# Performance work log

Measured on AMD Instinct MI355X. Metric: run time of the kernel, lower is better.

The kernel has to match this reference:

```python
import jax, jax.numpy as jnp
import numpy as np

D_MODEL = 2048
NUM_HEADS = 32
NUM_GROUPS = 8
D_K = D_MODEL // NUM_HEADS          # 64
HPG = NUM_HEADS // NUM_GROUPS       # heads per group = 4
B, S = 2, 2048


def setup_inputs() -> dict:
    key = jax.random.key(0)
    ks = jax.random.split(key, 9)
    w_scale = 0.02
    kv_dim = NUM_GROUPS * D_K
    return {
        "x":  jax.random.normal(ks[0], (B, S, D_MODEL), dtype=jnp.float32),
        "Wq": jax.random.normal(ks[1], (D_MODEL, D_MODEL), dtype=jnp.float32) * w_scale,
        "bq": jnp.zeros((D_MODEL,), dtype=jnp.float32),
        "Wk": jax.random.normal(ks[2], (D_MODEL, kv_dim), dtype=jnp.float32) * w_scale,
        "bk": jnp.zeros((kv_dim,), dtype=jnp.float32),
        "Wv": jax.random.normal(ks[3], (D_MODEL, kv_dim), dtype=jnp.float32) * w_scale,
        "bv": jnp.zeros((kv_dim,), dtype=jnp.float32),
        "Wo": jax.random.normal(ks[4], (D_MODEL, D_MODEL), dtype=jnp.float32) * w_scale,
        "bo": jnp.zeros((D_MODEL,), dtype=jnp.float32),
    }


def reference(x, Wq, bq, Wk, bk, Wv, bv, Wo, bo):
    b, s, _ = x.shape
    # projections (torch Linear math: x @ W^T + b, here weights stored as (in,out))
    Q = (x @ Wq + bq).reshape(b, s, NUM_HEADS, D_K).transpose(0, 2, 1, 3)   # [B,H,S,dk]
    Kg = (x @ Wk + bk).reshape(b, s, NUM_GROUPS, D_K).transpose(0, 2, 1, 3)  # [B,G,S,dk]
    Vg = (x @ Wv + bv).reshape(b, s, NUM_GROUPS, D_K).transpose(0, 2, 1, 3)
    # repeat_interleave K/V over head dim to full head count
    K = jnp.repeat(Kg, HPG, axis=1)  # [B,H,S,dk]
    V = jnp.repeat(Vg, HPG, axis=1)
    scores = jnp.einsum("bhqd,bhkd->bhqk", Q, K) / np.sqrt(D_K).astype(np.float32)
    attn = jax.nn.softmax(scores, axis=-1)
    out = jnp.einsum("bhqk,bhkd->bhqd", attn, V)               # [B,H,S,dk]
    out = out.transpose(0, 2, 1, 3).reshape(b, s, D_MODEL)
    out = out @ Wo + bo
    # module returns grouped K,V cache: K[:, ::HPG] == Kg
    return out, (Kg, Vg)
```

## Files before the change

### kernel.cpp

```cpp
#include <hip/hip_runtime.h>
#include <hip/hip_bf16.h>
#include <stdint.h>

#define S_LEN 2048
#define DM    2048
#define NH    32
#define NG    8
#define DK    64
#define BATCH 2
#define MROWS (BATCH*S_LEN)
#define NQKV  3072
#define SSCALE 0.18033688f

typedef __bf16 bf16x8 __attribute__((ext_vector_type(8)));
typedef short  s16x8  __attribute__((ext_vector_type(8)));
typedef float  f32x4  __attribute__((ext_vector_type(4)));
typedef unsigned int u32x4 __attribute__((ext_vector_type(4)));

__device__ __forceinline__ unsigned short f2b(float f) {
    unsigned int x = __float_as_uint(f);
    unsigned int r = (x + 0x7fffu + ((x >> 16) & 1u)) >> 16;
    return (unsigned short)r;
}
__device__ __forceinline__ bf16x8 ld8(const unsigned short* p) {
    return *(const bf16x8*)p;
}
__device__ __forceinline__ s16x8 cvt8(const float* p) {
    f32x4 a = *(const f32x4*)p;
    f32x4 b = *(const f32x4*)(p + 4);
    s16x8 o;
#pragma unroll
    for (int j = 0; j < 4; j++) { o[j] = (short)f2b(a[j]); o[4 + j] = (short)f2b(b[j]); }
    return o;
}
__device__ __forceinline__ void gl_lds(const unsigned short* g, unsigned short* l) {
    __builtin_amdgcn_global_load_lds(
        (const __attribute__((address_space(1))) unsigned int*)g,
        (__attribute__((address_space(3))) unsigned int*)l, 16, 0, 0);
}
__device__ __forceinline__ void wait_dma() {
    asm volatile("s_waitcnt vmcnt(0)" ::: "memory");
}

__global__ __launch_bounds__(256) void cvt_x(const float* __restrict__ in,
                                             unsigned short* __restrict__ out) {
    size_t id = (size_t)blockIdx.x * 256 + threadIdx.x;
    *(s16x8*)&out[id * 8] = cvt8(in + id * 8);
}

__global__ void transpose_cvt(const float* __restrict__ in,
                              unsigned short* __restrict__ out, int R, int C) {
    __shared__ float t[32][33];
    int c0 = blockIdx.x * 32, r0 = blockIdx.y * 32;
    int tx = threadIdx.x, ty = threadIdx.y;
#pragma unroll
    for (int i = 0; i < 4; i++)
        t[ty + i * 8][tx] = in[(size_t)(r0 + ty + i * 8) * C + c0 + tx];
    __syncthreads();
#pragma unroll
    for (int i = 0; i < 4; i++)
        out[(size_t)(c0 + ty + i * 8) * R + r0 + tx] = f2b(t[tx][ty + i * 8]);
}

__global__ void bias_concat(const float* __restrict__ bq, const float* __restrict__ bk,
                            const float* __restrict__ bv, float* __restrict__ o) {
    int i = blockIdx.x * 256 + threadIdx.x;
    if (i < 2048) o[i] = bq[i];
    else if (i < 2560) o[i] = bk[i - 2048];
    else if (i < 3072) o[i] = bv[i - 2560];
}

__global__ __launch_bounds__(256, 4) void gemm_qkv(const unsigned short* __restrict__ A,
                                                const unsigned short* __restrict__ Bt,
                                                const float* __restrict__ bias,
                                                unsigned short* __restrict__ Qb,
                                                float* __restrict__ Kg, float* __restrict__ Vg,
                                                unsigned short* __restrict__ Kb,
                                                unsigned short* __restrict__ Vtb) {
    __shared__ alignas(16) unsigned short As[2][128 * 32];
    __shared__ alignas(16) unsigned short Bs[2][128 * 32];
    const int K = DM;
    const int tid = threadIdx.x;
    const int n0 = blockIdx.x * 128, m0 = blockIdx.y * 128;
    const int w = tid >> 6, lane = tid & 63;
    const int ln15 = lane & 15, quad = lane >> 4;
    const int wm = (w >> 1) * 64, wn = (w & 1) * 64;
    const int xq = (quad ^ ((ln15 >> 1) & 3)) * 8;
    f32x4 acc[4][4] = {};

#define GSTAGE(k0v, buf) do {                                                    \
    _Pragma("unroll")                                                            \
    for (int i = 0; i < 2; ++i) {                                                \
        int s = w * 128 + i * 64 + lane;             \
        int r = s >> 2, cb = (s & 3) ^ ((r >> 1) & 3);                           \
        gl_lds(&A[(size_t)(m0 + r) * K + (k0v) + cb * 8],                        \
               &As[buf][(w * 128 + i * 64) * 8]);                                \
        gl_lds(&Bt[(size_t)(n0 + r) * K + (k0v) + cb * 8],                       \
               &Bs[buf][(w * 128 + i * 64) * 8]);                                \
    } } while (0)

    GSTAGE(0, 0);
    wait_dma();
    __syncthreads();
    int cur = 0;
    for (int k0 = 0; k0 < K; k0 += 32) {
        if (k0 + 32 < K) GSTAGE(k0 + 32, cur ^ 1);
        bf16x8 af[4], bfr[4];
#pragma unroll
        for (int mt = 0; mt < 4; mt++)
            af[mt] = ld8(&As[cur][(wm + mt * 16 + ln15) * 32 + xq]);
#pragma unroll
        for (int nt = 0; nt < 4; nt++)
            bfr[nt] = ld8(&Bs[cur][(wn + nt * 16 + ln15) * 32 + xq]);
        __builtin_amdgcn_s_setprio(1);
#pragma unroll
        for (int mt = 0; mt < 4; mt++)
#pragma unroll
            for (int nt = 0; nt < 4; nt++)
                acc[mt][nt] = __builtin_amdgcn_mfma_f32_16x16x32_bf16(af[mt], bfr[nt], acc[mt][nt], 0, 0, 0);
        __builtin_amdgcn_s_setprio(0);
        wait_dma();
        __syncthreads();
        cur ^= 1;
    }
#undef GSTAGE
#pragma unroll
    for (int nt = 0; nt < 4; nt++) {
        int col = n0 + wn + nt * 16 + ln15;
        float bv = bias[col];
#pragma unroll
        for (int mt = 0; mt < 4; mt++) {
            int row0 = m0 + wm + mt * 16 + quad * 4;
#pragma unroll
            for (int r = 0; r < 4; r++) {
                float val = acc[mt][nt][r] + bv;
                int row = row0 + r;
                int b = row >> 11, s = row & 2047;
                if (col < 2048) {
                    Qb[(size_t)row * DM + col] = f2b(val * SSCALE);
                } else if (col < 2560) {
                    int gc = col - 2048, g = gc >> 6, d = gc & 63;
                    size_t idx = (((size_t)(b * NG + g) * S_LEN + s) << 6) + d;
                    Kg[idx] = val;
                    Kb[idx] = f2b(val);
                } else {
                    int gc = col - 2560, g = gc >> 6, d = gc & 63;
                    Vg[(((size_t)(b * NG + g) * S_LEN + s) << 6) + d] = val;
                    Vtb[((size_t)(b * NG + g) * DK + d) * S_LEN + s] = f2b(val);
                }
            }
        }
    }
}

__global__ __launch_bounds__(256, 4) void gemm_o(const unsigned short* __restrict__ A,
                                              const unsigned short* __restrict__ Bt,
                                              const float* __restrict__ bias,
                                              float* __restrict__ C) {
    __shared__ alignas(16) unsigned short As[2][128 * 32];
    __shared__ alignas(16) unsigned short Bs[2][128 * 32];
    const int K = DM, N = DM;
    const int tid = threadIdx.x;
    const int n0 = blockIdx.x * 128, m0 = blockIdx.y * 128;
    const int w = tid >> 6, lane = tid & 63;
    const int ln15 = lane & 15, quad = lane >> 4;
    const int wm = (w >> 1) * 64, wn = (w & 1) * 64;
    const int xq = (quad ^ ((ln15 >> 1) & 3)) * 8;
    f32x4 acc[4][4] = {};

#define GSTAGE(k0v, buf) do {                                                    \
    _Pragma("unroll")                                                            \
    for (int i = 0; i < 2; ++i) {                                                \
        int s = w * 128 + i * 64 + lane;                                         \
        int r = s >> 2, cb = (s & 3) ^ ((r >> 1) & 3);                           \
        gl_lds(&A[(size_t)(m0 + r) * K + (k0v) + cb * 8],                        \
               &As[buf][(w * 128 + i * 64) * 8]);                                \
        gl_lds(&Bt[(size_t)(n0 + r) * K + (k0v) + cb * 8],                       \
               &Bs[buf][(w * 128 + i * 64) * 8]);                                \
    } } while (0)

    GSTAGE(0, 0);
    wait_dma();
    __syncthreads();
    int cur = 0;
    for (int k0 = 0; k0 < K; k0 += 32) {
        if (k0 + 32 < K) GSTAGE(k0 + 32, cur ^ 1);
        bf16x8 af[4], bfr[4];
#pragma unroll
        for (int mt = 0; mt < 4; mt++)
            af[mt] = ld8(&As[cur][(wm + mt * 16 + ln15) * 32 + xq]);
#pragma unroll
        for (int nt = 0; nt < 4; nt++)
            bfr[nt] = ld8(&Bs[cur][(wn + nt * 16 + ln15) * 32 + xq]);
        __builtin_amdgcn_s_setprio(1);
#pragma unroll
        for (int mt = 0; mt < 4; mt++)
#pragma unroll
            for (int nt = 0; nt < 4; nt++)
                acc[mt][nt] = __builtin_amdgcn_mfma_f32_16x16x32_bf16(af[mt], bfr[nt], acc[mt][nt], 0, 0, 0);
        __builtin_amdgcn_s_setprio(0);
        wait_dma();
        __syncthreads();
        cur ^= 1;
    }
#undef GSTAGE
#pragma unroll
    for (int nt = 0; nt < 4; nt++) {
        int col = n0 + wn + nt * 16 + ln15;
        float bv = bias[col];
#pragma unroll
        for (int mt = 0; mt < 4; mt++) {
            int row0 = m0 + wm + mt * 16 + quad * 4;
#pragma unroll
            for (int r = 0; r < 4; r++)
                C[(size_t)(row0 + r) * N + col] = acc[mt][nt][r] + bv;
        }
    }
}

#define MT 2
__global__ __launch_bounds__(256, 4) void attn_fwd(const unsigned short* __restrict__ Qb,
                                                   const unsigned short* __restrict__ Kb,
                                                   const unsigned short* __restrict__ Vtb,
                                                   unsigned short* __restrict__ AO) {
    __shared__ alignas(16) unsigned short Ks[2][64 * 64];
    __shared__ alignas(16) unsigned short Vt[2][64 * 64];
    const int b = blockIdx.z, h = blockIdx.y, q0 = blockIdx.x * (MT * 64);
    const int g = h >> 2;
    const int tid = threadIdx.x;
    const int w = tid >> 6, lane = tid & 63;
    const int ln15 = lane & 15, quad = lane >> 4;
    const int x7a = (quad ^ (ln15 & 7)) * 8;
    const int x7b = x7a ^ 32;

    bf16x8 aq[MT][2];
#pragma unroll
    for (int mt = 0; mt < MT; mt++) {
        const size_t qrow =
            ((size_t)(b * S_LEN + q0 + w * (MT * 16) + mt * 16 + ln15)) * DM + h * DK;
        aq[mt][0] = ld8(&Qb[qrow + quad * 8]);
        aq[mt][1] = ld8(&Qb[qrow + 32 + quad * 8]);
    }

    bf16x8 ones;
#pragma unroll
    for (int j = 0; j < 8; j++) ones[j] = (__bf16)1.0f;

    f32x4 o[MT][4] = {};
    f32x4 l_acc[MT] = {};
    const size_t kvb = ((size_t)(b * NG + g)) * S_LEN * DK;

#define STAGE(k0v, buf) do {                                                     \
    _Pragma("unroll")                                                            \
    for (int i = 0; i < 2; i++) {                                                \
        int s = w * 128 + i * 64 + lane;                                         \
        int r = s >> 3, cb = (s & 7) ^ (r & 7);                                  \
        gl_lds(&Kb[kvb + (size_t)((k0v) + r) * DK + cb * 8],                     \
               &Ks[buf][(w * 128 + i * 64) * 8]);                                \
        gl_lds(&Vtb[kvb + (size_t)r * S_LEN + (k0v) + cb * 8],                   \
               &Vt[buf][(w * 128 + i * 64) * 8]);                                \
    } } while (0)

    STAGE(0, 0);
    wait_dma();
    __syncthreads();
    int cur = 0;

    for (int k0 = 0; k0 < S_LEN; k0 += 64) {
        if (k0 + 64 < S_LEN) STAGE(k0 + 64, cur ^ 1);

        f32x4 z[MT][4];
        __builtin_amdgcn_s_setprio(1);
#pragma unroll
        for (int nt = 0; nt < 4; nt++) {
            bf16x8 bk0 = ld8(&Ks[cur][(nt * 16 + ln15) * 64 + x7a]);
            bf16x8 bk1 = ld8(&Ks[cur][(nt * 16 + ln15) * 64 + x7b]);
#pragma unroll
            for (int mt = 0; mt < MT; mt++) {
                f32x4 t = {0.f, 0.f, 0.f, 0.f};
                t = __builtin_amdgcn_mfma_f32_16x16x32_bf16(bk0, aq[mt][0], t, 0, 0, 0);
                t = __builtin_amdgcn_mfma_f32_16x16x32_bf16(bk1, aq[mt][1], t, 0, 0, 0);
                z[mt][nt] = t;
            }
        }
        __builtin_amdgcn_s_setprio(0);

        bf16x8 pa[MT][2];
#pragma unroll
        for (int mt = 0; mt < MT; mt++) {
            unsigned int S[4][2];
#pragma unroll
            for (int nt = 0; nt < 4; nt++) {
                f32x4 pe;
#pragma unroll
                for (int r = 0; r < 4; r++)
                    pe[r] = __builtin_amdgcn_exp2f(z[mt][nt][r]);
                asm("v_cvt_pk_bf16_f32 %0, %1, %2" : "=v"(S[nt][0]) : "v"(pe[0]), "v"(pe[1]));
                asm("v_cvt_pk_bf16_f32 %0, %1, %2" : "=v"(S[nt][1]) : "v"(pe[2]), "v"(pe[3]));
            }
#pragma unroll
            for (int f = 0; f < 2; f++) {
                unsigned int wA[2], wB[2];
#pragma unroll
                for (int p = 0; p < 2; p++) {
                    unsigned int xa = S[2 * f][p], yb = S[2 * f + 1][p];
                    asm("v_permlane32_swap_b32 %0, %1" : "+v"(xa), "+v"(yb));
                    asm("v_permlane16_swap_b32 %0, %1" : "+v"(xa), "+v"(yb));
                    wA[p] = xa; wB[p] = yb;
                }
                u32x4 t4;
                t4[0] = wA[0]; t4[1] = wA[1]; t4[2] = wB[0]; t4[3] = wB[1];
                pa[mt][f] = __builtin_bit_cast(bf16x8, t4);
            }
        }

        __builtin_amdgcn_s_setprio(1);
#pragma unroll
        for (int nt = 0; nt < 4; nt++) {
            bf16x8 bv0 = ld8(&Vt[cur][(nt * 16 + ln15) * 64 + x7a]);
            bf16x8 bv1 = ld8(&Vt[cur][(nt * 16 + ln15) * 64 + x7b]);
#pragma unroll
            for (int mt = 0; mt < MT; mt++) {
                f32x4 t = o[mt][nt];
                t = __builtin_amdgcn_mfma_f32_16x16x32_bf16(pa[mt][0], bv0, t, 0, 0, 0);
                t = __builtin_amdgcn_mfma_f32_16x16x32_bf16(pa[mt][1], bv1, t, 0, 0, 0);
                o[mt][nt] = t;
            }
        }
#pragma unroll
        for (int mt = 0; mt < MT; mt++) {
            l_acc[mt] = __builtin_amdgcn_mfma_f32_16x16x32_bf16(pa[mt][0], ones, l_acc[mt], 0, 0, 0);
            l_acc[mt] = __builtin_amdgcn_mfma_f32_16x16x32_bf16(pa[mt][1], ones, l_acc[mt], 0, 0, 0);
        }
        __builtin_amdgcn_s_setprio(0);

        wait_dma();
        __syncthreads();
        cur ^= 1;
    }
#undef STAGE

#pragma unroll
    for (int mt = 0; mt < MT; mt++) {
#pragma unroll
        for (int r = 0; r < 4; r++) {
            float inv = 1.0f / l_acc[mt][r];
            int q = q0 + w * (MT * 16) + mt * 16 + quad * 4 + r;
#pragma unroll
            for (int nt = 0; nt < 4; nt++) {
                int col = h * DK + nt * 16 + ln15;
                *(__bf16*)&AO[((size_t)(b * S_LEN + q)) * DM + col] =
                    (__bf16)(o[mt][nt][r] * inv);
            }
        }
    }
}

extern "C" void kernel_launch(void* const* d_in, const int* in_sizes, int n_in,
                              void* d_out, int out_size, void* d_ws, size_t ws_size,
                              hipStream_t stream) {
    const float* x  = (const float*)d_in[0];
    const float* Wq = (const float*)d_in[1];
    const float* bq = (const float*)d_in[2];
    const float* Wk = (const float*)d_in[3];
    const float* bk = (const float*)d_in[4];
    const float* Wv = (const float*)d_in[5];
    const float* bv = (const float*)d_in[6];
    const float* Wo = (const float*)d_in[7];
    const float* bo = (const float*)d_in[8];

    float* out = (float*)d_out;
    float* Kg  = out + (size_t)MROWS * DM;
    float* Vg  = Kg + (size_t)BATCH * NG * S_LEN * DK;

    unsigned short* Qb = (unsigned short*)d_out;

    unsigned short* ws    = (unsigned short*)d_ws;
    unsigned short* WqkvT = ws;
    unsigned short* WoT   = WqkvT + (size_t)NQKV * DM;
    unsigned short* Kb    = WoT + (size_t)DM * DM;
    unsigned short* Vtb   = Kb + (size_t)BATCH * NG * S_LEN * DK;
    unsigned short* AO    = Vtb + (size_t)BATCH * NG * S_LEN * DK;
    unsigned short* xb    = AO + (size_t)MROWS * DM;
    float*          bqkv  = (float*)(xb + (size_t)MROWS * DM);

    hipLaunchKernelGGL(cvt_x, dim3(MROWS * DM / 8 / 256), dim3(256), 0, stream, x, xb);

    dim3 tb(32, 8);
    hipLaunchKernelGGL(transpose_cvt, dim3(DM / 32, DM / 32), tb, 0, stream,
                       Wq, WqkvT, DM, DM);
    hipLaunchKernelGGL(transpose_cvt, dim3(512 / 32, DM / 32), tb, 0, stream,
                       Wk, WqkvT + (size_t)2048 * DM, DM, 512);
    hipLaunchKernelGGL(transpose_cvt, dim3(512 / 32, DM / 32), tb, 0, stream,
                       Wv, WqkvT + (size_t)2560 * DM, DM, 512);
    hipLaunchKernelGGL(transpose_cvt, dim3(DM / 32, DM / 32), tb, 0, stream,
                       Wo, WoT, DM, DM);
    hipLaunchKernelGGL(bias_concat, dim3(12), dim3(256), 0, stream, bq, bk, bv, bqkv);

    hipLaunchKernelGGL(gemm_qkv, dim3(NQKV / 128, MROWS / 128), dim3(256), 0, stream,
                       xb, WqkvT, bqkv, Qb, Kg, Vg, Kb, Vtb);

    hipLaunchKernelGGL(attn_fwd, dim3(S_LEN / (MT * 64), NH, BATCH), dim3(256), 0, stream,
                       Qb, Kb, Vtb, AO);

    hipLaunchKernelGGL(gemm_o, dim3(DM / 128, MROWS / 128), dim3(256), 0, stream,
                       AO, WoT, bo, out);
}
```

Baseline: 326.9 us.

## Triple-buffer GEMM and attention loads and fuse prep kernels into one launch

```diff
diff --git a/kernel.cpp b/kernel.cpp
--- a/kernel.cpp
+++ b/kernel.cpp
@@ -38,21 +38,58 @@
         (const __attribute__((address_space(1))) unsigned int*)g,
         (__attribute__((address_space(3))) unsigned int*)l, 16, 0, 0);
 }
-__device__ __forceinline__ void wait_dma() {
+__device__ __forceinline__ void wait_vm4() {
+    asm volatile("s_waitcnt vmcnt(4)" ::: "memory");
+}
+__device__ __forceinline__ void wait_vm0() {
     asm volatile("s_waitcnt vmcnt(0)" ::: "memory");
 }
-
-__global__ __launch_bounds__(256) void cvt_x(const float* __restrict__ in,
-                                             unsigned short* __restrict__ out) {
-    size_t id = (size_t)blockIdx.x * 256 + threadIdx.x;
-    *(s16x8*)&out[id * 8] = cvt8(in + id * 8);
-}
-
-__global__ void transpose_cvt(const float* __restrict__ in,
-                              unsigned short* __restrict__ out, int R, int C) {
+__device__ __forceinline__ void bar() {
+    __builtin_amdgcn_sched_barrier(0);
+    __builtin_amdgcn_s_barrier();
+    __builtin_amdgcn_sched_barrier(0);
+}
+
+#define TCVT 4096
+#define TQ   4096
+#define TK   1024
+#define TV   1024
+#define TO   4096
+#define TB   12
+#define NPREP (TCVT+TQ+TK+TV+TO+TB)
+__global__ __launch_bounds__(256) void prep_fused(
+    const float* __restrict__ x,
+    const float* __restrict__ Wq, const float* __restrict__ Wk,
+    const float* __restrict__ Wv, const float* __restrict__ Wo,
+    const float* __restrict__ bq, const float* __restrict__ bk,
+    const float* __restrict__ bv,
+    unsigned short* __restrict__ xb,
+    unsigned short* __restrict__ WqkvT, unsigned short* __restrict__ WoT,
+    float* __restrict__ bqkv) {
     __shared__ float t[32][33];
-    int c0 = blockIdx.x * 32, r0 = blockIdx.y * 32;
-    int tx = threadIdx.x, ty = threadIdx.y;
+    int bid = blockIdx.x;
+    const int tx = threadIdx.x, ty = threadIdx.y;
+    const int flat = ty * 32 + tx;
+    if (bid < TCVT) {
+        size_t id = (size_t)bid * 256 + flat;
+        *(s16x8*)&xb[id * 8] = cvt8(x + id * 8);
+        return;
+    }
+    bid -= TCVT;
+    const float* in; unsigned short* out; int C, bx, by;
+    if (bid < TQ) { in = Wq; out = WqkvT; C = DM; bx = bid & 63; by = bid >> 6; }
+    else if ((bid -= TQ) < TK) { in = Wk; out = WqkvT + (size_t)2048 * DM; C = 512; bx = bid & 15; by = bid >> 4; }
+    else if ((bid -= TK) < TV) { in = Wv; out = WqkvT + (size_t)2560 * DM; C = 512; bx = bid & 15; by = bid >> 4; }
+    else if ((bid -= TV) < TO) { in = Wo; out = WoT; C = DM; bx = bid & 63; by = bid >> 6; }
+    else {
+        int i = (bid - TO) * 256 + flat;
+        if (i < 2048) bqkv[i] = bq[i];
+        else if (i < 2560) bqkv[i] = bk[i - 2048];
+        else if (i < 3072) bqkv[i] = bv[i - 2560];
+        return;
+    }
+    const int R = DM;
+    int c0 = bx * 32, r0 = by * 32;
 #pragma unroll
     for (int i = 0; i < 4; i++)
         t[ty + i * 8][tx] = in[(size_t)(r0 + ty + i * 8) * C + c0 + tx];
@@ -62,23 +99,15 @@
         out[(size_t)(c0 + ty + i * 8) * R + r0 + tx] = f2b(t[tx][ty + i * 8]);
 }
 
-__global__ void bias_concat(const float* __restrict__ bq, const float* __restrict__ bk,
-                            const float* __restrict__ bv, float* __restrict__ o) {
-    int i = blockIdx.x * 256 + threadIdx.x;
-    if (i < 2048) o[i] = bq[i];
-    else if (i < 2560) o[i] = bk[i - 2048];
-    else if (i < 3072) o[i] = bv[i - 2560];
-}
-
-__global__ __launch_bounds__(256, 4) void gemm_qkv(const unsigned short* __restrict__ A,
+__global__ __launch_bounds__(256, 3) void gemm_qkv(const unsigned short* __restrict__ A,
                                                 const unsigned short* __restrict__ Bt,
                                                 const float* __restrict__ bias,
                                                 unsigned short* __restrict__ Qb,
                                                 float* __restrict__ Kg, float* __restrict__ Vg,
                                                 unsigned short* __restrict__ Kb,
                                                 unsigned short* __restrict__ Vtb) {
-    __shared__ alignas(16) unsigned short As[2][128 * 32];
-    __shared__ alignas(16) unsigned short Bs[2][128 * 32];
+    __shared__ alignas(16) unsigned short As[3][128 * 32];
+    __shared__ alignas(16) unsigned short Bs[3][128 * 32];
     const int K = DM;
     const int tid = threadIdx.x;
     const int n0 = blockIdx.x * 128, m0 = blockIdx.y * 128;
@@ -100,11 +129,15 @@
     } } while (0)
 
     GSTAGE(0, 0);
-    wait_dma();
-    __syncthreads();
+    GSTAGE(32, 1);
     int cur = 0;
     for (int k0 = 0; k0 < K; k0 += 32) {
-        if (k0 + 32 < K) GSTAGE(k0 + 32, cur ^ 1);
+        if (k0 + 32 < K) wait_vm4(); else wait_vm0();
+        bar();
+        if (k0 + 64 < K) {
+            int nb = cur + 2; if (nb >= 3) nb -= 3;
+            GSTAGE(k0 + 64, nb);
+        }
         bf16x8 af[4], bfr[4];
 #pragma unroll
         for (int mt = 0; mt < 4; mt++)
@@ -119,9 +152,7 @@
             for (int nt = 0; nt < 4; nt++)
                 acc[mt][nt] = __builtin_amdgcn_mfma_f32_16x16x32_bf16(af[mt], bfr[nt], acc[mt][nt], 0, 0, 0);
         __builtin_amdgcn_s_setprio(0);
-        wait_dma();
-        __syncthreads();
-        cur ^= 1;
+        cur = (cur + 1 == 3) ? 0 : cur + 1;
     }
 #undef GSTAGE
 #pragma unroll
@@ -153,12 +184,12 @@
     }
 }
 
-__global__ __launch_bounds__(256, 4) void gemm_o(const unsigned short* __restrict__ A,
+__global__ __launch_bounds__(256, 3) void gemm_o(const unsigned short* __restrict__ A,
                                               const unsigned short* __restrict__ Bt,
                                               const float* __restrict__ bias,
                                               float* __restrict__ C) {
-    __shared__ alignas(16) unsigned short As[2][128 * 32];
-    __shared__ alignas(16) unsigned short Bs[2][128 * 32];
+    __shared__ alignas(16) unsigned short As[3][128 * 32];
+    __shared__ alignas(16) unsigned short Bs[3][128 * 32];
     const int K = DM, N = DM;
     const int tid = threadIdx.x;
     const int n0 = blockIdx.x * 128, m0 = blockIdx.y * 128;
@@ -180,11 +211,15 @@
     } } while (0)
 
     GSTAGE(0, 0);
-    wait_dma();
-    __syncthreads();
+    GSTAGE(32, 1);
     int cur = 0;
     for (int k0 = 0; k0 < K; k0 += 32) {
-        if (k0 + 32 < K) GSTAGE(k0 + 32, cur ^ 1);
+        if (k0 + 32 < K) wait_vm4(); else wait_vm0();
+        bar();
+        if (k0 + 64 < K) {
+            int nb = cur + 2; if (nb >= 3) nb -= 3;
+            GSTAGE(k0 + 64, nb);
+        }
         bf16x8 af[4], bfr[4];
 #pragma unroll
         for (int mt = 0; mt < 4; mt++)
@@ -199,9 +234,7 @@
             for (int nt = 0; nt < 4; nt++)
                 acc[mt][nt] = __builtin_amdgcn_mfma_f32_16x16x32_bf16(af[mt], bfr[nt], acc[mt][nt], 0, 0, 0);
         __builtin_amdgcn_s_setprio(0);
-        wait_dma();
-        __syncthreads();
-        cur ^= 1;
+        cur = (cur + 1 == 3) ? 0 : cur + 1;
     }
 #undef GSTAGE
 #pragma unroll
@@ -219,12 +252,12 @@
 }
 
 #define MT 2
-__global__ __launch_bounds__(256, 4) void attn_fwd(const unsigned short* __restrict__ Qb,
+__global__ __launch_bounds__(256, 3) void attn_fwd(const unsigned short* __restrict__ Qb,
                                                    const unsigned short* __restrict__ Kb,
                                                    const unsigned short* __restrict__ Vtb,
                                                    unsigned short* __restrict__ AO) {
-    __shared__ alignas(16) unsigned short Ks[2][64 * 64];
-    __shared__ alignas(16) unsigned short Vt[2][64 * 64];
+    __shared__ alignas(16) unsigned short Ks[3][64 * 64];
+    __shared__ alignas(16) unsigned short Vt[3][64 * 64];
     const int b = blockIdx.z, h = blockIdx.y, q0 = blockIdx.x * (MT * 64);
     const int g = h >> 2;
     const int tid = threadIdx.x;
@@ -262,12 +295,16 @@
     } } while (0)
 
     STAGE(0, 0);
-    wait_dma();
-    __syncthreads();
+    STAGE(64, 1);
     int cur = 0;
 
     for (int k0 = 0; k0 < S_LEN; k0 += 64) {
-        if (k0 + 64 < S_LEN) STAGE(k0 + 64, cur ^ 1);
+        if (k0 + 64 < S_LEN) wait_vm4(); else wait_vm0();
+        bar();
+        if (k0 + 128 < S_LEN) {
+            int nb = cur + 2; if (nb >= 3) nb -= 3;
+            STAGE(k0 + 128, nb);
+        }
 
         f32x4 z[MT][4];
         __builtin_amdgcn_s_setprio(1);
@@ -334,9 +371,7 @@
         }
         __builtin_amdgcn_s_setprio(0);
 
-        wait_dma();
-        __syncthreads();
-        cur ^= 1;
+        cur = (cur + 1 == 3) ? 0 : cur + 1;
     }
 #undef STAGE
 
@@ -384,18 +419,8 @@
     unsigned short* xb    = AO + (size_t)MROWS * DM;
     float*          bqkv  = (float*)(xb + (size_t)MROWS * DM);
 
-    hipLaunchKernelGGL(cvt_x, dim3(MROWS * DM / 8 / 256), dim3(256), 0, stream, x, xb);
-
-    dim3 tb(32, 8);
-    hipLaunchKernelGGL(transpose_cvt, dim3(DM / 32, DM / 32), tb, 0, stream,
-                       Wq, WqkvT, DM, DM);
-    hipLaunchKernelGGL(transpose_cvt, dim3(512 / 32, DM / 32), tb, 0, stream,
-                       Wk, WqkvT + (size_t)2048 * DM, DM, 512);
-    hipLaunchKernelGGL(transpose_cvt, dim3(512 / 32, DM / 32), tb, 0, stream,
-                       Wv, WqkvT + (size_t)2560 * DM, DM, 512);
-    hipLaunchKernelGGL(transpose_cvt, dim3(DM / 32, DM / 32), tb, 0, stream,
-                       Wo, WoT, DM, DM);
-    hipLaunchKernelGGL(bias_concat, dim3(12), dim3(256), 0, stream, bq, bk, bv, bqkv);
+    hipLaunchKernelGGL(prep_fused, dim3(NPREP), dim3(32, 8), 0, stream,
+                       x, Wq, Wk, Wv, Wo, bq, bk, bv, xb, WqkvT, WoT, bqkv);
 
     hipLaunchKernelGGL(gemm_qkv, dim3(NQKV / 128, MROWS / 128), dim3(256), 0, stream,
                        xb, WqkvT, bqkv, Qb, Kg, Vg, Kb, Vtb);
```

Result: no change. 327.2 us (+0.1%).
